# Kernel optimization log

Measured on AMD Instinct MI355X. Metric: run time of the kernel, lower is better.

## Reference

```python
import jax, jax.numpy as jnp
import numpy as np

VOCAB, EMBED, ZCH = 4096, 128, 256
B, H, W = 32, 16, 16


def setup_inputs() -> dict:
    key = jax.random.key(0)
    k1, k2, k3, k4 = jax.random.split(key, 4)
    z_e = jax.random.normal(k1, (B, ZCH, H, W), dtype=jnp.float32)
    pre_w = jax.random.normal(k2, (EMBED, ZCH), dtype=jnp.float32) * 0.02
    pre_b = jnp.zeros((EMBED,), dtype=jnp.float32)
    # codebook initialized uniform(-1/vocab, 1/vocab) like the torch module
    emb = jax.random.uniform(k3, (VOCAB, EMBED), dtype=jnp.float32,
                             minval=-1.0 / VOCAB, maxval=1.0 / VOCAB)
    post_w = jax.random.normal(k4, (ZCH, EMBED), dtype=jnp.float32) * 0.02
    post_b = jnp.zeros((ZCH,), dtype=jnp.float32)
    return {"z_e": z_e, "pre_w": pre_w, "pre_b": pre_b, "emb": emb,
            "post_w": post_w, "post_b": post_b}


def reference(z_e, pre_w, pre_b, emb, post_w, post_b):
    # pre_quant_conv: 1x1 conv == per-pixel linear, z_channels -> embed_dim
    z = jnp.einsum('bchw,ec->behw', z_e, pre_w) + pre_b[None, :, None, None]
    b, e, h, w = z.shape
    zf = z.transpose(0, 2, 3, 1).reshape(-1, e)                 # (b*h*w, e)
    # squared distance to all codebook vectors: |z|^2 + |c|^2 - 2 z.c
    dist = (jnp.sum(zf * zf, axis=1, keepdims=True)
            + jnp.sum(emb * emb, axis=1)
            - 2.0 * zf @ emb.T)                                  # (b*h*w, vocab)
    tokens = jnp.argmin(dist, axis=-1)                           # (b*h*w,)
    z_q = emb[tokens].reshape(b, h, w, e).transpose(0, 3, 1, 2)  # (b,e,h,w)
    # straight-through estimator
    dec_in = z + jax.lax.stop_gradient(z_q - z)
    # post_quant_conv: 1x1 conv embed_dim -> z_channels (decoder input)
    rec = jnp.einsum('behw,ce->bchw', dec_in, post_w) + post_b[None, :, None, None]
    return z, z_q, rec
```

## Files before the change

### kernel.cpp

```cpp
#include <hip/hip_runtime.h>
#include <hip/hip_bf16.h>
#include <cstdint>

#define NB   32
#define NC   256
#define NE   128
#define NS   256
#define NV   4096
#define NP   8192
#define NSPLIT 8

typedef unsigned short ushort_t;
typedef __attribute__((ext_vector_type(8))) short bf16x8;
typedef __attribute__((ext_vector_type(8))) unsigned short us8;
typedef __attribute__((ext_vector_type(4))) float f32x4;

__device__ __forceinline__ float bf2f(ushort_t u) {
    union { unsigned int i; float f; } x; x.i = ((unsigned int)u) << 16; return x.f;
}
__device__ __forceinline__ ushort_t f2bf(float f) {
    __hip_bfloat16 h = __float2bfloat16(f);
    ushort_t u; __builtin_memcpy(&u, &h, 2); return u;
}
__device__ __forceinline__ unsigned asu(float f) { unsigned u; __builtin_memcpy(&u,&f,4); return u; }
__device__ __forceinline__ float    asf(unsigned u) { float f; __builtin_memcpy(&f,&u,4); return f; }

__global__ __launch_bounds__(256) void pre_conv_pack(
    const float* __restrict__ z_e, const float* __restrict__ pre_w,
    const float* __restrict__ pre_b, const float* __restrict__ emb,
    float* __restrict__ out_z, ushort_t* __restrict__ Bpack,
    float* __restrict__ cnorm)
{
    __shared__ __align__(16) float wtile[16 * 256];
    __shared__ __align__(16) float part[4 * 16 * 64];

    const int t = threadIdx.x;

    if (blockIdx.x == 8) {
        const int v     = (blockIdx.y * 4 + blockIdx.z) * 32 + (t >> 3);
        const int chunk = t & 7;
        const float4* rp = (const float4*)(emb + (size_t)v * NE + chunk * 16);
        float4 x0 = rp[0], x1 = rp[1], x2 = rp[2], x3 = rp[3];
        float xs[16] = { x0.x, x0.y, x0.z, x0.w, x1.x, x1.y, x1.z, x1.w,
                         x2.x, x2.y, x2.z, x2.w, x3.x, x3.y, x3.z, x3.w };
        us8 h0, h1;
        float nn = 0.f;
#pragma unroll
        for (int j = 0; j < 8; j++) {
            nn = fmaf(xs[j], xs[j], nn);
            h0[j] = f2bf(xs[j]);
        }
#pragma unroll
        for (int j = 0; j < 8; j++) {
            nn = fmaf(xs[8 + j], xs[8 + j], nn);
            h1[j] = f2bf(xs[8 + j]);
        }
        nn += __shfl_xor(nn, 1);
        nn += __shfl_xor(nn, 2);
        nn += __shfl_xor(nn, 4);
        if (chunk == 0) cnorm[v] = 0.5f * nn;

        const int G  = v >> 4;
        const int ks = chunk >> 1;
        const int q0 = (chunk & 1) * 2;
        const int L0 = (v & 15) | (q0 << 4);
        const int L1 = (v & 15) | ((q0 + 1) << 4);
        *(us8*)(Bpack + ((size_t)G * 4 + ks) * 512 + L0 * 8) = h0;
        *(us8*)(Bpack + ((size_t)G * 4 + ks) * 512 + L1 * 8) = h1;
        return;
    }

    const int e0 = blockIdx.x * 16;
    const int b  = blockIdx.y;
    const int s0 = blockIdx.z * 64;

    for (int idx = t; idx < 16 * 256; idx += 256)
        wtile[idx] = pre_w[(e0 + (idx >> 8)) * 256 + (idx & 255)];
    __syncthreads();

    const int kq = t >> 6, sl = t & 63;
    float acc[16];
#pragma unroll
    for (int r = 0; r < 16; r++) acc[r] = 0.f;

    const float* zin = z_e + (size_t)(b * NC + kq * 64) * NS + s0 + sl;
    const int cb = kq * 64;
#pragma unroll 4
    for (int i = 0; i < 16; i++) {
        const int c = i * 4;
        float z0 = zin[(c + 0) * NS];
        float z1 = zin[(c + 1) * NS];
        float z2 = zin[(c + 2) * NS];
        float z3 = zin[(c + 3) * NS];
#pragma unroll
        for (int r = 0; r < 16; r++) {
            float4 w = *(const float4*)&wtile[r * 256 + cb + c];
            acc[r] = fmaf(z0, w.x, fmaf(z1, w.y, fmaf(z2, w.z, fmaf(z3, w.w, acc[r]))));
        }
    }
#pragma unroll
    for (int r = 0; r < 16; r++)
        part[(kq * 16 + r) * 64 + sl] = acc[r];
    __syncthreads();

    const int r4 = t >> 6, sl2 = t & 63;
#pragma unroll
    for (int j = 0; j < 4; j++) {
        const int r = j * 4 + r4;
        float v = pre_b[e0 + r]
                + part[(0 * 16 + r) * 64 + sl2]
                + part[(1 * 16 + r) * 64 + sl2]
                + part[(2 * 16 + r) * 64 + sl2]
                + part[(3 * 16 + r) * 64 + sl2];
        out_z[(size_t)(b * NE + e0 + r) * NS + s0 + sl2] = v;
    }
}

__global__ __launch_bounds__(256, 3) void score_mfma(
    const float* __restrict__ z, const ushort_t* __restrict__ Bpack,
    const float* __restrict__ cnorm, int* __restrict__ pidx4)
{
    __shared__ __align__(16) char smraw[40960];
    float* As  = (float*)smraw;
    float* r1  = (float*)smraw;
    float* r2  = (float*)(smraw + 16640);
    float* t4b = (float*)(smraw + 33280);

    const int t = threadIdx.x;
    const int wave = t >> 6, lane = t & 63;
    const int set = blockIdx.x;
    const int split = blockIdx.y;
    const int p0 = set * 64;
    const int b  = p0 >> 8;
    const int s0 = p0 & 255;

    for (int idx = t; idx < 64 * 128; idx += 256) {
        int k = idx >> 6, i = idx & 63;
        As[i * 132 + k] = z[(size_t)(b * NE + k) * NS + s0 + i];
    }
    __syncthreads();

    const int am = lane & 15, aq = lane >> 4;
    bf16x8 ah[4][4];
#pragma unroll
    for (int mt = 0; mt < 4; mt++)
#pragma unroll
        for (int ks = 0; ks < 4; ks++) {
            const unsigned* src = (const unsigned*)(As + (mt * 16 + am) * 132 + ks * 32 + aq * 8);
            union { unsigned u[4]; bf16x8 v; } pk;
#pragma unroll
            for (int pr = 0; pr < 4; pr++)
                pk.u[pr] = (src[2 * pr + 1] & 0xFFFF0000u) | (src[2 * pr] >> 16);
            ah[mt][ks] = pk.v;
        }
    __syncthreads();

    const int Gbase = split * 32 + wave * 8;
    float cn[8];
#pragma unroll
    for (int cgi = 0; cgi < 8; cgi++)
        cn[cgi] = cnorm[(Gbase + cgi) * 16 + am];

    float b1v[16], b2v[16];
#pragma unroll
    for (int i = 0; i < 16; i++) { b1v[i] = -1e30f; b2v[i] = -1e30f; }

    bf16x8 bh[4], bhn[4];
#pragma unroll
    for (int ks = 0; ks < 4; ks++)
        bh[ks] = *(const bf16x8*)(Bpack + ((size_t)Gbase * 4 + ks) * 512 + lane * 8);

    for (int cgi = 0; cgi < 8; cgi++) {
        if (cgi < 7) {
#pragma unroll
            for (int ks = 0; ks < 4; ks++)
                bhn[ks] = *(const bf16x8*)(Bpack + ((size_t)(Gbase + cgi + 1) * 4 + ks) * 512 + lane * 8);
        }

        f32x4 acc[4];
#pragma unroll
        for (int mt = 0; mt < 4; mt++) acc[mt] = (f32x4){0.f, 0.f, 0.f, 0.f};
#pragma unroll
        for (int ks = 0; ks < 4; ks++)
#pragma unroll
            for (int mt = 0; mt < 4; mt++)
                acc[mt] = __builtin_amdgcn_mfma_f32_16x16x32_bf16(ah[mt][ks], bh[ks], acc[mt], 0, 0, 0);

#pragma unroll
        for (int mt = 0; mt < 4; mt++)
#pragma unroll
            for (int reg = 0; reg < 4; reg++) {
                const int si = mt * 4 + reg;
                float sc = acc[mt][reg] - cn[cgi];
                float ev = asf((asu(sc) & ~7u) | (unsigned)cgi);
                b2v[si] = fmaxf(b2v[si], fminf(ev, b1v[si]));
                b1v[si] = fmaxf(b1v[si], ev);
            }
#pragma unroll
        for (int ks = 0; ks < 4; ks++) bh[ks] = bhn[ks];
    }

    const int slot = wave * 16 + am;
#pragma unroll
    for (int mt = 0; mt < 4; mt++)
#pragma unroll
        for (int reg = 0; reg < 4; reg++) {
            int px = mt * 16 + aq * 4 + reg;
            r1[slot * 65 + px] = b1v[mt * 4 + reg];
            r2[slot * 65 + px] = b2v[mt * 4 + reg];
        }
    __syncthreads();

    {
        const int px = t >> 2, ch = t & 3;
        float t1 = -1e30f, t2 = -1e30f, t3 = -1e30f, t4 = -1e30f;
        for (int i = 0; i < 16; i++) {
            int sl = ch * 16 + i;
#pragma unroll
            for (int e = 0; e < 2; e++) {
                float raw = e ? r2[sl * 65 + px] : r1[sl * 65 + px];
                unsigned vb = asu(raw);
                float v = asf((vb & ~511u) | ((unsigned)sl << 3) | (vb & 7u));
                t4 = fmaxf(t4, fminf(v, t3));
                t3 = fmaxf(t3, fminf(v, t2));
                t2 = fmaxf(t2, fminf(v, t1));
                t1 = fmaxf(t1, v);
            }
        }
        float* dst = t4b + (px * 4 + ch) * 4;
        dst[0] = t1; dst[1] = t2; dst[2] = t3; dst[3] = t4;
    }
    __syncthreads();

    if (t < 64) {
        float u1 = -1e30f, u2 = -1e30f, u3 = -1e30f, u4 = -1e30f;
        for (int ch = 0; ch < 4; ch++) {
#pragma unroll
            for (int j = 0; j < 4; j++) {
                float v = t4b[(t * 4 + ch) * 4 + j];
                u4 = fmaxf(u4, fminf(v, u3));
                u3 = fmaxf(u3, fminf(v, u2));
                u2 = fmaxf(u2, fminf(v, u1));
                u1 = fmaxf(u1, v);
            }
        }
        const int p = p0 + t;
        float uu[4] = { u1, u2, u3, u4 };
#pragma unroll
        for (int j = 0; j < 4; j++) {
            unsigned bits = asu(uu[j]) & 511u;
            int w = (int)(bits >> 7), res = (int)((bits >> 3) & 15u), cg = (int)(bits & 7u);
            pidx4[((size_t)split * NP + p) * 4 + j] = split * 512 + (w * 8 + cg) * 16 + res;
        }
    }
}

__global__ __launch_bounds__(512, 4) void rescore_gather_post2(
    const float* __restrict__ z, const float* __restrict__ emb,
    const int* __restrict__ pidx4, const float* __restrict__ post_w,
    const float* __restrict__ post_b, float* __restrict__ out_zq,
    float* __restrict__ out_rec)
{
    __shared__ __align__(16) float zl[16 * 132];
    __shared__ __align__(16) float eg[16 * 132];
    __shared__ int tok[16];

    const int t  = threadIdx.x;
    const int p0 = blockIdx.x * 16;
    const int b  = p0 >> 8;
    const int s0 = p0 & 255;

    for (int idx = t; idx < 16 * 128; idx += 512) {
        int k = idx >> 4, i = idx & 15;
        zl[i * 132 + k] = z[(size_t)(b * NE + k) * NS + s0 + i];
    }
    __syncthreads();

    {
        const int il = t >> 5;
        const int cc = t & 31;
        const int p  = p0 + il;
        const int split = cc >> 2, slot = cc & 3;
        const int idx = pidx4[((size_t)split * NP + p) * 4 + slot];
        const float* er = emb + (size_t)idx * NE;
        const float* zr = &zl[il * 132];

        double d0 = 0.0, d1 = 0.0, d2 = 0.0, d3 = 0.0;
        double n0 = 0.0, n1 = 0.0, n2 = 0.0, n3 = 0.0;
#pragma unroll
        for (int k = 0; k < NE; k += 16) {
            float4 e0 = *(const float4*)(er + k + 0);
            float4 e1 = *(const float4*)(er + k + 4);
            float4 e2 = *(const float4*)(er + k + 8);
            float4 e3 = *(const float4*)(er + k + 12);
            float4 z0 = *(const float4*)(zr + k + 0);
            float4 z1 = *(const float4*)(zr + k + 4);
            float4 z2 = *(const float4*)(zr + k + 8);
            float4 z3 = *(const float4*)(zr + k + 12);
            d0 += (double)z0.x * e0.x; d0 += (double)z0.y * e0.y;
            d0 += (double)z0.z * e0.z; d0 += (double)z0.w * e0.w;
            d1 += (double)z1.x * e1.x; d1 += (double)z1.y * e1.y;
            d1 += (double)z1.z * e1.z; d1 += (double)z1.w * e1.w;
            d2 += (double)z2.x * e2.x; d2 += (double)z2.y * e2.y;
            d2 += (double)z2.z * e2.z; d2 += (double)z2.w * e2.w;
            d3 += (double)z3.x * e3.x; d3 += (double)z3.y * e3.y;
            d3 += (double)z3.z * e3.z; d3 += (double)z3.w * e3.w;
            n0 += (double)e0.x * e0.x; n0 += (double)e0.y * e0.y;
            n0 += (double)e0.z * e0.z; n0 += (double)e0.w * e0.w;
            n1 += (double)e1.x * e1.x; n1 += (double)e1.y * e1.y;
            n1 += (double)e1.z * e1.z; n1 += (double)e1.w * e1.w;
            n2 += (double)e2.x * e2.x; n2 += (double)e2.y * e2.y;
            n2 += (double)e2.z * e2.z; n2 += (double)e2.w * e2.w;
            n3 += (double)e3.x * e3.x; n3 += (double)e3.y * e3.y;
            n3 += (double)e3.z * e3.z; n3 += (double)e3.w * e3.w;
        }
        double bs = ((d0 + d1) + (d2 + d3)) - 0.5 * ((n0 + n1) + (n2 + n3));
        int bi = idx;
#pragma unroll
        for (int m = 1; m <= 16; m <<= 1) {
            double osc = __shfl_xor(bs, m);
            int    obi = __shfl_xor(bi, m);
            if (osc > bs || (osc == bs && obi < bi)) { bs = osc; bi = obi; }
        }
        if (cc == 0) tok[il] = bi;
    }
    __syncthreads();

    for (int idx = t; idx < NE * 16; idx += 512) {
        int e = idx >> 4, i = idx & 15;
        float v = emb[(size_t)tok[i] * NE + e];
        out_zq[(size_t)(b * NE + e) * NS + s0 + i] = v;
        eg[i * 132 + e] = v;
    }
    __syncthreads();

    {
        const int c  = t & 255;
        const int ph = t >> 8;
        const int pb = ph * 8;
        const float* wr = post_w + (size_t)c * NE;

        float a0 = 0.f, a1 = 0.f, a2 = 0.f, a3 = 0.f;
        float a4 = 0.f, a5 = 0.f, a6 = 0.f, a7 = 0.f;
#pragma unroll 4
        for (int k = 0; k < NE; k += 4) {
            float4 w4 = *(const float4*)(wr + k);
            float4 q;
            q = *(const float4*)&eg[(pb + 0) * 132 + k];
            a0 = fmaf(w4.x, q.x, fmaf(w4.y, q.y, fmaf(w4.z, q.z, fmaf(w4.w, q.w, a0))));
            q = *(const float4*)&eg[(pb + 1) * 132 + k];
            a1 = fmaf(w4.x, q.x, fmaf(w4.y, q.y, fmaf(w4.z, q.z, fmaf(w4.w, q.w, a1))));
            q = *(const float4*)&eg[(pb + 2) * 132 + k];
            a2 = fmaf(w4.x, q.x, fmaf(w4.y, q.y, fmaf(w4.z, q.z, fmaf(w4.w, q.w, a2))));
            q = *(const float4*)&eg[(pb + 3) * 132 + k];
            a3 = fmaf(w4.x, q.x, fmaf(w4.y, q.y, fmaf(w4.z, q.z, fmaf(w4.w, q.w, a3))));
            q = *(const float4*)&eg[(pb + 4) * 132 + k];
            a4 = fmaf(w4.x, q.x, fmaf(w4.y, q.y, fmaf(w4.z, q.z, fmaf(w4.w, q.w, a4))));
            q = *(const float4*)&eg[(pb + 5) * 132 + k];
            a5 = fmaf(w4.x, q.x, fmaf(w4.y, q.y, fmaf(w4.z, q.z, fmaf(w4.w, q.w, a5))));
            q = *(const float4*)&eg[(pb + 6) * 132 + k];
            a6 = fmaf(w4.x, q.x, fmaf(w4.y, q.y, fmaf(w4.z, q.z, fmaf(w4.w, q.w, a6))));
            q = *(const float4*)&eg[(pb + 7) * 132 + k];
            a7 = fmaf(w4.x, q.x, fmaf(w4.y, q.y, fmaf(w4.z, q.z, fmaf(w4.w, q.w, a7))));
        }
        const float bias = post_b[c];
        float4 lo = { a0 + bias, a1 + bias, a2 + bias, a3 + bias };
        float4 hi = { a4 + bias, a5 + bias, a6 + bias, a7 + bias };
        float* dst = out_rec + (size_t)(b * NC + c) * NS + s0 + pb;
        *(float4*)(dst + 0) = lo;
        *(float4*)(dst + 4) = hi;
    }
}

extern "C" void kernel_launch(void* const* d_in, const int* in_sizes, int n_in,
                              void* d_out, int out_size, void* d_ws, size_t ws_size,
                              hipStream_t stream)
{
    const float* z_e    = (const float*)d_in[0];
    const float* pre_w  = (const float*)d_in[1];
    const float* pre_b  = (const float*)d_in[2];
    const float* emb    = (const float*)d_in[3];
    const float* post_w = (const float*)d_in[4];
    const float* post_b = (const float*)d_in[5];

    float* out     = (float*)d_out;
    float* out_z   = out;
    float* out_zq  = out + 1048576;
    float* out_rec = out + 2097152;

    const size_t SZ_BPACK = (size_t)256 * 4 * 512 * 2;
    const size_t SZ_CNORM = (size_t)NV * 4;
    const size_t SZ_PIDX4 = (size_t)NSPLIT * NP * 4 * 4;
    const size_t NEED = SZ_BPACK + SZ_CNORM + SZ_PIDX4;
    char* scr = (ws_size >= NEED) ? (char*)d_ws : (char*)out_rec;
    ushort_t* Bpack = (ushort_t*)scr;
    float*    cnorm = (float*)(scr + SZ_BPACK);
    int*      pidx4 = (int*)(scr + SZ_BPACK + SZ_CNORM);

    pre_conv_pack       <<<dim3(9, 32, 4),    256, 0, stream>>>(z_e, pre_w, pre_b, emb,
                                                                out_z, Bpack, cnorm);
    score_mfma          <<<dim3(128, NSPLIT), 256, 0, stream>>>(out_z, Bpack, cnorm, pidx4);
    rescore_gather_post2<<<dim3(512),         512, 0, stream>>>(out_z, emb, pidx4,
                                                                post_w, post_b,
                                                                out_zq, out_rec);
}
```

Before: 152.9 us.

## Fuse pre-conv, codebook scoring, rescoring and post-conv into one per-tile kernel

Replaces the three-kernel pipeline with a small codebook-packing kernel and one fused kernel per 32-pixel tile. That kernel computes the pre-conv into shared memory, runs the bf16 MFMA scoring over all codebook splits in sequence, reduces the top-4 candidates per split in shared memory, rescores them in double precision, gathers, and applies the post-conv. It removes the global round trips of z and the candidate buffer and two launches. The cost is only 256 blocks, each looping serially over all 4096 codes, so parallelism across the GPU drops.

Measured after the change: 144.4 us. -5.5%, faster.

```diff
diff --git a/kernel.cpp b/kernel.cpp
--- a/kernel.cpp
+++ b/kernel.cpp
@@ -15,9 +15,6 @@
 typedef __attribute__((ext_vector_type(8))) unsigned short us8;
 typedef __attribute__((ext_vector_type(4))) float f32x4;
 
-__device__ __forceinline__ float bf2f(ushort_t u) {
-    union { unsigned int i; float f; } x; x.i = ((unsigned int)u) << 16; return x.f;
-}
 __device__ __forceinline__ ushort_t f2bf(float f) {
     __hip_bfloat16 h = __float2bfloat16(f);
     ushort_t u; __builtin_memcpy(&u, &h, 2); return u;
@@ -25,299 +22,305 @@
 __device__ __forceinline__ unsigned asu(float f) { unsigned u; __builtin_memcpy(&u,&f,4); return u; }
 __device__ __forceinline__ float    asf(unsigned u) { float f; __builtin_memcpy(&f,&u,4); return f; }
 
-__global__ __launch_bounds__(256) void pre_conv_pack(
+__global__ __launch_bounds__(256) void pack_emb(
+    const float* __restrict__ emb, ushort_t* __restrict__ Bpack,
+    float* __restrict__ cnorm)
+{
+    const int t = threadIdx.x;
+    const int v     = blockIdx.x * 32 + (t >> 3);
+    const int chunk = t & 7;
+    const float4* rp = (const float4*)(emb + (size_t)v * NE + chunk * 16);
+    float4 x0 = rp[0], x1 = rp[1], x2 = rp[2], x3 = rp[3];
+    float xs[16] = { x0.x, x0.y, x0.z, x0.w, x1.x, x1.y, x1.z, x1.w,
+                     x2.x, x2.y, x2.z, x2.w, x3.x, x3.y, x3.z, x3.w };
+    us8 h0, h1;
+    float nn = 0.f;
+#pragma unroll
+    for (int j = 0; j < 8; j++) {
+        nn = fmaf(xs[j], xs[j], nn);
+        h0[j] = f2bf(xs[j]);
+    }
+#pragma unroll
+    for (int j = 0; j < 8; j++) {
+        nn = fmaf(xs[8 + j], xs[8 + j], nn);
+        h1[j] = f2bf(xs[8 + j]);
+    }
+    nn += __shfl_xor(nn, 1);
+    nn += __shfl_xor(nn, 2);
+    nn += __shfl_xor(nn, 4);
+    if (chunk == 0) cnorm[v] = 0.5f * nn;
+
+    const int G  = v >> 4;
+    const int ks = chunk >> 1;
+    const int q0 = (chunk & 1) * 2;
+    const int L0 = (v & 15) | (q0 << 4);
+    const int L1 = (v & 15) | ((q0 + 1) << 4);
+    *(us8*)(Bpack + ((size_t)G * 4 + ks) * 512 + L0 * 8) = h0;
+    *(us8*)(Bpack + ((size_t)G * 4 + ks) * 512 + L1 * 8) = h1;
+}
+
+#define ZE_STR  36
+#define ZL_STR  132
+#define ZE_OFF  0
+#define R1_OFF  0
+#define R2_OFF  16896
+#define ZL_OFF  36864
+#define T4B_OFF 53760
+#define CAND_OFF 57856
+#define TOK_OFF 61952
+#define SM_SIZE 62080
+
+__global__ __launch_bounds__(512, 2) void vq_main(
     const float* __restrict__ z_e, const float* __restrict__ pre_w,
     const float* __restrict__ pre_b, const float* __restrict__ emb,
-    float* __restrict__ out_z, ushort_t* __restrict__ Bpack,
-    float* __restrict__ cnorm)
+    const float* __restrict__ post_w, const float* __restrict__ post_b,
+    const ushort_t* __restrict__ Bpack, const float* __restrict__ cnorm,
+    float* __restrict__ out_z, float* __restrict__ out_zq,
+    float* __restrict__ out_rec)
 {
-    __shared__ __align__(16) float wtile[16 * 256];
-    __shared__ __align__(16) float part[4 * 16 * 64];
-
-    const int t = threadIdx.x;
-
-    if (blockIdx.x == 8) {
-        const int v     = (blockIdx.y * 4 + blockIdx.z) * 32 + (t >> 3);
-        const int chunk = t & 7;
-        const float4* rp = (const float4*)(emb + (size_t)v * NE + chunk * 16);
-        float4 x0 = rp[0], x1 = rp[1], x2 = rp[2], x3 = rp[3];
-        float xs[16] = { x0.x, x0.y, x0.z, x0.w, x1.x, x1.y, x1.z, x1.w,
-                         x2.x, x2.y, x2.z, x2.w, x3.x, x3.y, x3.z, x3.w };
-        us8 h0, h1;
-        float nn = 0.f;
-#pragma unroll
-        for (int j = 0; j < 8; j++) {
-            nn = fmaf(xs[j], xs[j], nn);
-            h0[j] = f2bf(xs[j]);
-        }
-#pragma unroll
-        for (int j = 0; j < 8; j++) {
-            nn = fmaf(xs[8 + j], xs[8 + j], nn);
-            h1[j] = f2bf(xs[8 + j]);
-        }
-        nn += __shfl_xor(nn, 1);
-        nn += __shfl_xor(nn, 2);
-        nn += __shfl_xor(nn, 4);
-        if (chunk == 0) cnorm[v] = 0.5f * nn;
-
-        const int G  = v >> 4;
-        const int ks = chunk >> 1;
-        const int q0 = (chunk & 1) * 2;
-        const int L0 = (v & 15) | (q0 << 4);
-        const int L1 = (v & 15) | ((q0 + 1) << 4);
-        *(us8*)(Bpack + ((size_t)G * 4 + ks) * 512 + L0 * 8) = h0;
-        *(us8*)(Bpack + ((size_t)G * 4 + ks) * 512 + L1 * 8) = h1;
-        return;
-    }
-
-    const int e0 = blockIdx.x * 16;
-    const int b  = blockIdx.y;
-    const int s0 = blockIdx.z * 64;
-
-    for (int idx = t; idx < 16 * 256; idx += 256)
-        wtile[idx] = pre_w[(e0 + (idx >> 8)) * 256 + (idx & 255)];
+    __shared__ __align__(16) char smraw[SM_SIZE];
+    float* ze   = (float*)(smraw + ZE_OFF);
+    float* r1   = (float*)(smraw + R1_OFF);
+    float* r2   = (float*)(smraw + R2_OFF);
+    float* zl   = (float*)(smraw + ZL_OFF);
+    float* eg   = (float*)(smraw + ZL_OFF);
+    float* t4b  = (float*)(smraw + T4B_OFF);
+    int*   cand = (int*)(smraw + CAND_OFF);
+    int*   tok  = (int*)(smraw + TOK_OFF);
+
+    const int t  = threadIdx.x;
+    const int b  = blockIdx.x >> 3;
+    const int s0 = (blockIdx.x & 7) * 32;
+
+    for (int idx = t; idx < NC * 32; idx += 512) {
+        int c = idx >> 5, i = idx & 31;
+        ze[c * ZE_STR + i] = z_e[((size_t)b * NC + c) * NS + s0 + i];
+    }
     __syncthreads();
 
-    const int kq = t >> 6, sl = t & 63;
-    float acc[16];
-#pragma unroll
-    for (int r = 0; r < 16; r++) acc[r] = 0.f;
-
-    const float* zin = z_e + (size_t)(b * NC + kq * 64) * NS + s0 + sl;
-    const int cb = kq * 64;
-#pragma unroll 4
-    for (int i = 0; i < 16; i++) {
-        const int c = i * 4;
-        float z0 = zin[(c + 0) * NS];
-        float z1 = zin[(c + 1) * NS];
-        float z2 = zin[(c + 2) * NS];
-        float z3 = zin[(c + 3) * NS];
-#pragma unroll
-        for (int r = 0; r < 16; r++) {
-            float4 w = *(const float4*)&wtile[r * 256 + cb + c];
-            acc[r] = fmaf(z0, w.x, fmaf(z1, w.y, fmaf(z2, w.z, fmaf(z3, w.w, acc[r]))));
-        }
-    }
-#pragma unroll
-    for (int r = 0; r < 16; r++)
-        part[(kq * 16 + r) * 64 + sl] = acc[r];
+    {
+        const int pg = t >> 7;
+        const int e  = t & 127;
+        const float* wr = pre_w + (size_t)e * NC;
+        float a0 = 0.f, a1 = 0.f, a2 = 0.f, a3 = 0.f;
+        float a4 = 0.f, a5 = 0.f, a6 = 0.f, a7 = 0.f;
+#pragma unroll 2
+        for (int c = 0; c < NC; c += 4) {
+            float4 w4 = *(const float4*)(wr + c);
+            float4 za, zb;
+            za = *(const float4*)&ze[(c + 0) * ZE_STR + pg * 8];
+            zb = *(const float4*)&ze[(c + 0) * ZE_STR + pg * 8 + 4];
+            a0 = fmaf(w4.x, za.x, a0); a1 = fmaf(w4.x, za.y, a1);
+            a2 = fmaf(w4.x, za.z, a2); a3 = fmaf(w4.x, za.w, a3);
+            a4 = fmaf(w4.x, zb.x, a4); a5 = fmaf(w4.x, zb.y, a5);
+            a6 = fmaf(w4.x, zb.z, a6); a7 = fmaf(w4.x, zb.w, a7);
+            za = *(const float4*)&ze[(c + 1) * ZE_STR + pg * 8];
+            zb = *(const float4*)&ze[(c + 1) * ZE_STR + pg * 8 + 4];
+            a0 = fmaf(w4.y, za.x, a0); a1 = fmaf(w4.y, za.y, a1);
+            a2 = fmaf(w4.y, za.z, a2); a3 = fmaf(w4.y, za.w, a3);
+            a4 = fmaf(w4.y, zb.x, a4); a5 = fmaf(w4.y, zb.y, a5);
+            a6 = fmaf(w4.y, zb.z, a6); a7 = fmaf(w4.y, zb.w, a7);
+            za = *(const float4*)&ze[(c + 2) * ZE_STR + pg * 8];
+            zb = *(const float4*)&ze[(c + 2) * ZE_STR + pg * 8 + 4];
+            a0 = fmaf(w4.z, za.x, a0); a1 = fmaf(w4.z, za.y, a1);
+            a2 = fmaf(w4.z, za.z, a2); a3 = fmaf(w4.z, za.w, a3);
+            a4 = fmaf(w4.z, zb.x, a4); a5 = fmaf(w4.z, zb.y, a5);
+            a6 = fmaf(w4.z, zb.z, a6); a7 = fmaf(w4.z, zb.w, a7);
+            za = *(const float4*)&ze[(c + 3) * ZE_STR + pg * 8];
+            zb = *(const float4*)&ze[(c + 3) * ZE_STR + pg * 8 + 4];
+            a0 = fmaf(w4.w, za.x, a0); a1 = fmaf(w4.w, za.y, a1);
+            a2 = fmaf(w4.w, za.z, a2); a3 = fmaf(w4.w, za.w, a3);
+            a4 = fmaf(w4.w, zb.x, a4); a5 = fmaf(w4.w, zb.y, a5);
+            a6 = fmaf(w4.w, zb.z, a6); a7 = fmaf(w4.w, zb.w, a7);
+        }
+        const float bias = pre_b[e];
+        a0 += bias; a1 += bias; a2 += bias; a3 += bias;
+        a4 += bias; a5 += bias; a6 += bias; a7 += bias;
+        zl[(pg * 8 + 0) * ZL_STR + e] = a0;
+        zl[(pg * 8 + 1) * ZL_STR + e] = a1;
+        zl[(pg * 8 + 2) * ZL_STR + e] = a2;
+        zl[(pg * 8 + 3) * ZL_STR + e] = a3;
+        zl[(pg * 8 + 4) * ZL_STR + e] = a4;
+        zl[(pg * 8 + 5) * ZL_STR + e] = a5;
+        zl[(pg * 8 + 6) * ZL_STR + e] = a6;
+        zl[(pg * 8 + 7) * ZL_STR + e] = a7;
+        float4 lo = { a0, a1, a2, a3 };
+        float4 hi = { a4, a5, a6, a7 };
+        float* dst = out_z + ((size_t)b * NE + e) * NS + s0 + pg * 8;
+        *(float4*)(dst + 0) = lo;
+        *(float4*)(dst + 4) = hi;
+    }
     __syncthreads();
 
-    const int r4 = t >> 6, sl2 = t & 63;
-#pragma unroll
-    for (int j = 0; j < 4; j++) {
-        const int r = j * 4 + r4;
-        float v = pre_b[e0 + r]
-                + part[(0 * 16 + r) * 64 + sl2]
-                + part[(1 * 16 + r) * 64 + sl2]
-                + part[(2 * 16 + r) * 64 + sl2]
-                + part[(3 * 16 + r) * 64 + sl2];
-        out_z[(size_t)(b * NE + e0 + r) * NS + s0 + sl2] = v;
-    }
-}
-
-__global__ __launch_bounds__(256, 3) void score_mfma(
-    const float* __restrict__ z, const ushort_t* __restrict__ Bpack,
-    const float* __restrict__ cnorm, int* __restrict__ pidx4)
-{
-    __shared__ __align__(16) char smraw[40960];
-    float* As  = (float*)smraw;
-    float* r1  = (float*)smraw;
-    float* r2  = (float*)(smraw + 16640);
-    float* t4b = (float*)(smraw + 33280);
-
-    const int t = threadIdx.x;
     const int wave = t >> 6, lane = t & 63;
-    const int set = blockIdx.x;
-    const int split = blockIdx.y;
-    const int p0 = set * 64;
-    const int b  = p0 >> 8;
-    const int s0 = p0 & 255;
-
-    for (int idx = t; idx < 64 * 128; idx += 256) {
-        int k = idx >> 6, i = idx & 63;
-        As[i * 132 + k] = z[(size_t)(b * NE + k) * NS + s0 + i];
-    }
-    __syncthreads();
-
     const int am = lane & 15, aq = lane >> 4;
-    bf16x8 ah[4][4];
-#pragma unroll
-    for (int mt = 0; mt < 4; mt++)
+
+    bf16x8 ah[2][4];
+#pragma unroll
+    for (int mt = 0; mt < 2; mt++)
 #pragma unroll
         for (int ks = 0; ks < 4; ks++) {
-            const unsigned* src = (const unsigned*)(As + (mt * 16 + am) * 132 + ks * 32 + aq * 8);
+            const unsigned* src = (const unsigned*)(zl + (mt * 16 + am) * ZL_STR + ks * 32 + aq * 8);
             union { unsigned u[4]; bf16x8 v; } pk;
 #pragma unroll
             for (int pr = 0; pr < 4; pr++)
                 pk.u[pr] = (src[2 * pr + 1] & 0xFFFF0000u) | (src[2 * pr] >> 16);
             ah[mt][ks] = pk.v;
         }
-    __syncthreads();
-
-    const int Gbase = split * 32 + wave * 8;
-    float cn[8];
-#pragma unroll
-    for (int cgi = 0; cgi < 8; cgi++)
-        cn[cgi] = cnorm[(Gbase + cgi) * 16 + am];
-
-    float b1v[16], b2v[16];
-#pragma unroll
-    for (int i = 0; i < 16; i++) { b1v[i] = -1e30f; b2v[i] = -1e30f; }
-
-    bf16x8 bh[4], bhn[4];
-#pragma unroll
-    for (int ks = 0; ks < 4; ks++)
-        bh[ks] = *(const bf16x8*)(Bpack + ((size_t)Gbase * 4 + ks) * 512 + lane * 8);
-
-    for (int cgi = 0; cgi < 8; cgi++) {
-        if (cgi < 7) {
+
+    const int wq = wave >> 2;
+    const int wv = wave & 3;
+
+    for (int sp = 0; sp < NSPLIT; sp += 2) {
+        const int split = sp + wq;
+        const int Gbase = split * 32 + wv * 8;
+        float cn[8];
+#pragma unroll
+        for (int cgi = 0; cgi < 8; cgi++)
+            cn[cgi] = cnorm[(Gbase + cgi) * 16 + am];
+
+        float b1v[8], b2v[8];
+#pragma unroll
+        for (int i = 0; i < 8; i++) { b1v[i] = -1e30f; b2v[i] = -1e30f; }
+
+        bf16x8 bh[4], bhn[4];
+#pragma unroll
+        for (int ks = 0; ks < 4; ks++)
+            bh[ks] = *(const bf16x8*)(Bpack + ((size_t)Gbase * 4 + ks) * 512 + lane * 8);
+
+        for (int cgi = 0; cgi < 8; cgi++) {
+            if (cgi < 7) {
+#pragma unroll
+                for (int ks = 0; ks < 4; ks++)
+                    bhn[ks] = *(const bf16x8*)(Bpack + ((size_t)(Gbase + cgi + 1) * 4 + ks) * 512 + lane * 8);
+            }
+            f32x4 acc[2];
+#pragma unroll
+            for (int mt = 0; mt < 2; mt++) acc[mt] = (f32x4){0.f, 0.f, 0.f, 0.f};
 #pragma unroll
             for (int ks = 0; ks < 4; ks++)
-                bhn[ks] = *(const bf16x8*)(Bpack + ((size_t)(Gbase + cgi + 1) * 4 + ks) * 512 + lane * 8);
-        }
-
-        f32x4 acc[4];
-#pragma unroll
-        for (int mt = 0; mt < 4; mt++) acc[mt] = (f32x4){0.f, 0.f, 0.f, 0.f};
-#pragma unroll
-        for (int ks = 0; ks < 4; ks++)
-#pragma unroll
-            for (int mt = 0; mt < 4; mt++)
-                acc[mt] = __builtin_amdgcn_mfma_f32_16x16x32_bf16(ah[mt][ks], bh[ks], acc[mt], 0, 0, 0);
-
-#pragma unroll
-        for (int mt = 0; mt < 4; mt++)
+#pragma unroll
+                for (int mt = 0; mt < 2; mt++)
+                    acc[mt] = __builtin_amdgcn_mfma_f32_16x16x32_bf16(ah[mt][ks], bh[ks], acc[mt], 0, 0, 0);
+
+#pragma unroll
+            for (int mt = 0; mt < 2; mt++)
+#pragma unroll
+                for (int reg = 0; reg < 4; reg++) {
+                    const int si = mt * 4 + reg;
+                    float sc = acc[mt][reg] - cn[cgi];
+                    float ev = asf((asu(sc) & ~7u) | (unsigned)cgi);
+                    b2v[si] = fmaxf(b2v[si], fminf(ev, b1v[si]));
+                    b1v[si] = fmaxf(b1v[si], ev);
+                }
+#pragma unroll
+            for (int ks = 0; ks < 4; ks++) bh[ks] = bhn[ks];
+        }
+
+        const int slot = wv * 16 + am;
+#pragma unroll
+        for (int mt = 0; mt < 2; mt++)
 #pragma unroll
             for (int reg = 0; reg < 4; reg++) {
-                const int si = mt * 4 + reg;
-                float sc = acc[mt][reg] - cn[cgi];
-                float ev = asf((asu(sc) & ~7u) | (unsigned)cgi);
-                b2v[si] = fmaxf(b2v[si], fminf(ev, b1v[si]));
-                b1v[si] = fmaxf(b1v[si], ev);
-            }
-#pragma unroll
-        for (int ks = 0; ks < 4; ks++) bh[ks] = bhn[ks];
-    }
-
-    const int slot = wave * 16 + am;
-#pragma unroll
-    for (int mt = 0; mt < 4; mt++)
-#pragma unroll
-        for (int reg = 0; reg < 4; reg++) {
-            int px = mt * 16 + aq * 4 + reg;
-            r1[slot * 65 + px] = b1v[mt * 4 + reg];
-            r2[slot * 65 + px] = b2v[mt * 4 + reg];
-        }
-    __syncthreads();
+                int px = mt * 16 + aq * 4 + reg;
+                r1[(wq * 64 + slot) * 33 + px] = b1v[mt * 4 + reg];
+                r2[(wq * 64 + slot) * 33 + px] = b2v[mt * 4 + reg];
+            }
+        __syncthreads();
+
+        if (t < 256) {
+            const int wq2 = t >> 7, rem = t & 127;
+            const int px = rem >> 2, ch = rem & 3;
+            float t1 = -1e30f, t2 = -1e30f, t3 = -1e30f, t4 = -1e30f;
+            for (int i = 0; i < 16; i++) {
+                int sl = ch * 16 + i;
+#pragma unroll
+                for (int e = 0; e < 2; e++) {
+                    float raw = e ? r2[(wq2 * 64 + sl) * 33 + px]
+                                  : r1[(wq2 * 64 + sl) * 33 + px];
+                    unsigned vb = asu(raw);
+                    float v = asf((vb & ~511u) | ((unsigned)sl << 3) | (vb & 7u));
+                    t4 = fmaxf(t4, fminf(v, t3));
+                    t3 = fmaxf(t3, fminf(v, t2));
+                    t2 = fmaxf(t2, fminf(v, t1));
+                    t1 = fmaxf(t1, v);
+                }
+            }
+            float* dst = t4b + ((wq2 * 32 + px) * 4 + ch) * 4;
+            dst[0] = t1; dst[1] = t2; dst[2] = t3; dst[3] = t4;
+        }
+        __syncthreads();
+
+        if (t < 64) {
+            const int wq2 = t >> 5, px = t & 31;
+            float u1 = -1e30f, u2 = -1e30f, u3 = -1e30f, u4 = -1e30f;
+            for (int ch = 0; ch < 4; ch++) {
+#pragma unroll
+                for (int j = 0; j < 4; j++) {
+                    float v = t4b[((wq2 * 32 + px) * 4 + ch) * 4 + j];
+                    u4 = fmaxf(u4, fminf(v, u3));
+                    u3 = fmaxf(u3, fminf(v, u2));
+                    u2 = fmaxf(u2, fminf(v, u1));
+                    u1 = fmaxf(u1, v);
+                }
+            }
+            const int spw = sp + wq2;
+            float uu[4] = { u1, u2, u3, u4 };
+#pragma unroll
+            for (int j = 0; j < 4; j++) {
+                unsigned bits = asu(uu[j]) & 511u;
+                int w = (int)(bits >> 7), res = (int)((bits >> 3) & 15u), cg = (int)(bits & 7u);
+                cand[(spw * 32 + px) * 4 + j] = spw * 512 + (w * 8 + cg) * 16 + res;
+            }
+        }
+        __syncthreads();
+    }
 
     {
-        const int px = t >> 2, ch = t & 3;
-        float t1 = -1e30f, t2 = -1e30f, t3 = -1e30f, t4 = -1e30f;
-        for (int i = 0; i < 16; i++) {
-            int sl = ch * 16 + i;
-#pragma unroll
-            for (int e = 0; e < 2; e++) {
-                float raw = e ? r2[sl * 65 + px] : r1[sl * 65 + px];
-                unsigned vb = asu(raw);
-                float v = asf((vb & ~511u) | ((unsigned)sl << 3) | (vb & 7u));
-                t4 = fmaxf(t4, fminf(v, t3));
-                t3 = fmaxf(t3, fminf(v, t2));
-                t2 = fmaxf(t2, fminf(v, t1));
-                t1 = fmaxf(t1, v);
-            }
-        }
-        float* dst = t4b + (px * 4 + ch) * 4;
-        dst[0] = t1; dst[1] = t2; dst[2] = t3; dst[3] = t4;
-    }
-    __syncthreads();
-
-    if (t < 64) {
-        float u1 = -1e30f, u2 = -1e30f, u3 = -1e30f, u4 = -1e30f;
-        for (int ch = 0; ch < 4; ch++) {
-#pragma unroll
-            for (int j = 0; j < 4; j++) {
-                float v = t4b[(t * 4 + ch) * 4 + j];
-                u4 = fmaxf(u4, fminf(v, u3));
-                u3 = fmaxf(u3, fminf(v, u2));
-                u2 = fmaxf(u2, fminf(v, u1));
-                u1 = fmaxf(u1, v);
-            }
-        }
-        const int p = p0 + t;
-        float uu[4] = { u1, u2, u3, u4 };
-#pragma unroll
-        for (int j = 0; j < 4; j++) {
-            unsigned bits = asu(uu[j]) & 511u;
-            int w = (int)(bits >> 7), res = (int)((bits >> 3) & 15u), cg = (int)(bits & 7u);
-            pidx4[((size_t)split * NP + p) * 4 + j] = split * 512 + (w * 8 + cg) * 16 + res;
-        }
-    }
-}
-
-__global__ __launch_bounds__(512, 4) void rescore_gather_post2(
-    const float* __restrict__ z, const float* __restrict__ emb,
-    const int* __restrict__ pidx4, const float* __restrict__ post_w,
-    const float* __restrict__ post_b, float* __restrict__ out_zq,
-    float* __restrict__ out_rec)
-{
-    __shared__ __align__(16) float zl[16 * 132];
-    __shared__ __align__(16) float eg[16 * 132];
-    __shared__ int tok[16];
-
-    const int t  = threadIdx.x;
-    const int p0 = blockIdx.x * 16;
-    const int b  = p0 >> 8;
-    const int s0 = p0 & 255;
-
-    for (int idx = t; idx < 16 * 128; idx += 512) {
-        int k = idx >> 4, i = idx & 15;
-        zl[i * 132 + k] = z[(size_t)(b * NE + k) * NS + s0 + i];
-    }
-    __syncthreads();
-
-    {
-        const int il = t >> 5;
-        const int cc = t & 31;
-        const int p  = p0 + il;
-        const int split = cc >> 2, slot = cc & 3;
-        const int idx = pidx4[((size_t)split * NP + p) * 4 + slot];
-        const float* er = emb + (size_t)idx * NE;
-        const float* zr = &zl[il * 132];
-
-        double d0 = 0.0, d1 = 0.0, d2 = 0.0, d3 = 0.0;
-        double n0 = 0.0, n1 = 0.0, n2 = 0.0, n3 = 0.0;
-#pragma unroll
-        for (int k = 0; k < NE; k += 16) {
-            float4 e0 = *(const float4*)(er + k + 0);
-            float4 e1 = *(const float4*)(er + k + 4);
-            float4 e2 = *(const float4*)(er + k + 8);
-            float4 e3 = *(const float4*)(er + k + 12);
-            float4 z0 = *(const float4*)(zr + k + 0);
-            float4 z1 = *(const float4*)(zr + k + 4);
-            float4 z2 = *(const float4*)(zr + k + 8);
-            float4 z3 = *(const float4*)(zr + k + 12);
-            d0 += (double)z0.x * e0.x; d0 += (double)z0.y * e0.y;
-            d0 += (double)z0.z * e0.z; d0 += (double)z0.w * e0.w;
-            d1 += (double)z1.x * e1.x; d1 += (double)z1.y * e1.y;
-            d1 += (double)z1.z * e1.z; d1 += (double)z1.w * e1.w;
-            d2 += (double)z2.x * e2.x; d2 += (double)z2.y * e2.y;
-            d2 += (double)z2.z * e2.z; d2 += (double)z2.w * e2.w;
-            d3 += (double)z3.x * e3.x; d3 += (double)z3.y * e3.y;
-            d3 += (double)z3.z * e3.z; d3 += (double)z3.w * e3.w;
-            n0 += (double)e0.x * e0.x; n0 += (double)e0.y * e0.y;
-            n0 += (double)e0.z * e0.z; n0 += (double)e0.w * e0.w;
-            n1 += (double)e1.x * e1.x; n1 += (double)e1.y * e1.y;
-            n1 += (double)e1.z * e1.z; n1 += (double)e1.w * e1.w;
-            n2 += (double)e2.x * e2.x; n2 += (double)e2.y * e2.y;
-            n2 += (double)e2.z * e2.z; n2 += (double)e2.w * e2.w;
-            n3 += (double)e3.x * e3.x; n3 += (double)e3.y * e3.y;
-            n3 += (double)e3.z * e3.z; n3 += (double)e3.w * e3.w;
-        }
-        double bs = ((d0 + d1) + (d2 + d3)) - 0.5 * ((n0 + n1) + (n2 + n3));
-        int bi = idx;
-#pragma unroll
-        for (int m = 1; m <= 16; m <<= 1) {
+        const int il = t >> 4;
+        const int cc = t & 15;
+        double bs = -1e300; int bi = 0x7fffffff;
+        const float* zr = zl + il * ZL_STR;
+#pragma unroll
+        for (int jj = 0; jj < 2; jj++) {
+            int c2 = cc * 2 + jj;
+            int split = c2 >> 2, slot = c2 & 3;
+            int idx = cand[(split * 32 + il) * 4 + slot];
+            const float* er = emb + (size_t)idx * NE;
+            double d0 = 0.0, d1 = 0.0, d2 = 0.0, d3 = 0.0;
+            double n0 = 0.0, n1 = 0.0, n2 = 0.0, n3 = 0.0;
+#pragma unroll
+            for (int k = 0; k < NE; k += 16) {
+                float4 e0 = *(const float4*)(er + k + 0);
+                float4 e1 = *(const float4*)(er + k + 4);
+                float4 e2 = *(const float4*)(er + k + 8);
+                float4 e3 = *(const float4*)(er + k + 12);
+                float4 z0 = *(const float4*)(zr + k + 0);
+                float4 z1 = *(const float4*)(zr + k + 4);
+                float4 z2 = *(const float4*)(zr + k + 8);
+                float4 z3 = *(const float4*)(zr + k + 12);
+                d0 += (double)z0.x * e0.x; d0 += (double)z0.y * e0.y;
+                d0 += (double)z0.z * e0.z; d0 += (double)z0.w * e0.w;
+                d1 += (double)z1.x * e1.x; d1 += (double)z1.y * e1.y;
+                d1 += (double)z1.z * e1.z; d1 += (double)z1.w * e1.w;
+                d2 += (double)z2.x * e2.x; d2 += (double)z2.y * e2.y;
+                d2 += (double)z2.z * e2.z; d2 += (double)z2.w * e2.w;
+                d3 += (double)z3.x * e3.x; d3 += (double)z3.y * e3.y;
+                d3 += (double)z3.z * e3.z; d3 += (double)z3.w * e3.w;
+                n0 += (double)e0.x * e0.x; n0 += (double)e0.y * e0.y;
+                n0 += (double)e0.z * e0.z; n0 += (double)e0.w * e0.w;
+                n1 += (double)e1.x * e1.x; n1 += (double)e1.y * e1.y;
+                n1 += (double)e1.z * e1.z; n1 += (double)e1.w * e1.w;
+                n2 += (double)e2.x * e2.x; n2 += (double)e2.y * e2.y;
+                n2 += (double)e2.z * e2.z; n2 += (double)e2.w * e2.w;
+                n3 += (double)e3.x * e3.x; n3 += (double)e3.y * e3.y;
+                n3 += (double)e3.z * e3.z; n3 += (double)e3.w * e3.w;
+            }
+            double sc = ((d0 + d1) + (d2 + d3)) - 0.5 * ((n0 + n1) + (n2 + n3));
+            if (sc > bs || (sc == bs && idx < bi)) { bs = sc; bi = idx; }
+        }
+#pragma unroll
+        for (int m = 1; m <= 8; m <<= 1) {
             double osc = __shfl_xor(bs, m);
             int    obi = __shfl_xor(bi, m);
             if (osc > bs || (osc == bs && obi < bi)) { bs = osc; bi = obi; }
@@ -326,49 +329,55 @@
     }
     __syncthreads();
 
-    for (int idx = t; idx < NE * 16; idx += 512) {
-        int e = idx >> 4, i = idx & 15;
-        float v = emb[(size_t)tok[i] * NE + e];
-        out_zq[(size_t)(b * NE + e) * NS + s0 + i] = v;
-        eg[i * 132 + e] = v;
+    for (int idx = t; idx < 32 * 32; idx += 512) {
+        int px = idx >> 5, eq = idx & 31;
+        float4 v4 = *(const float4*)(emb + (size_t)tok[px] * NE + eq * 4);
+        *(float4*)&eg[px * ZL_STR + eq * 4] = v4;
+    }
+    __syncthreads();
+    for (int idx = t; idx < NE * 32; idx += 512) {
+        int e = idx >> 5, i = idx & 31;
+        out_zq[((size_t)b * NE + e) * NS + s0 + i] = eg[i * ZL_STR + e];
     }
     __syncthreads();
 
     {
         const int c  = t & 255;
         const int ph = t >> 8;
-        const int pb = ph * 8;
         const float* wr = post_w + (size_t)c * NE;
-
-        float a0 = 0.f, a1 = 0.f, a2 = 0.f, a3 = 0.f;
-        float a4 = 0.f, a5 = 0.f, a6 = 0.f, a7 = 0.f;
+        const float bias = post_b[c];
+#pragma unroll
+        for (int pass = 0; pass < 2; pass++) {
+            const int pb = pass * 16 + ph * 8;
+            float a0 = 0.f, a1 = 0.f, a2 = 0.f, a3 = 0.f;
+            float a4 = 0.f, a5 = 0.f, a6 = 0.f, a7 = 0.f;
 #pragma unroll 4
-        for (int k = 0; k < NE; k += 4) {
-            float4 w4 = *(const float4*)(wr + k);
-            float4 q;
-            q = *(const float4*)&eg[(pb + 0) * 132 + k];
-            a0 = fmaf(w4.x, q.x, fmaf(w4.y, q.y, fmaf(w4.z, q.z, fmaf(w4.w, q.w, a0))));
-            q = *(const float4*)&eg[(pb + 1) * 132 + k];
-            a1 = fmaf(w4.x, q.x, fmaf(w4.y, q.y, fmaf(w4.z, q.z, fmaf(w4.w, q.w, a1))));
-            q = *(const float4*)&eg[(pb + 2) * 132 + k];
-            a2 = fmaf(w4.x, q.x, fmaf(w4.y, q.y, fmaf(w4.z, q.z, fmaf(w4.w, q.w, a2))));
-            q = *(const float4*)&eg[(pb + 3) * 132 + k];
-            a3 = fmaf(w4.x, q.x, fmaf(w4.y, q.y, fmaf(w4.z, q.z, fmaf(w4.w, q.w, a3))));
-            q = *(const float4*)&eg[(pb + 4) * 132 + k];
-            a4 = fmaf(w4.x, q.x, fmaf(w4.y, q.y, fmaf(w4.z, q.z, fmaf(w4.w, q.w, a4))));
-            q = *(const float4*)&eg[(pb + 5) * 132 + k];
-            a5 = fmaf(w4.x, q.x, fmaf(w4.y, q.y, fmaf(w4.z, q.z, fmaf(w4.w, q.w, a5))));
-            q = *(const float4*)&eg[(pb + 6) * 132 + k];
-            a6 = fmaf(w4.x, q.x, fmaf(w4.y, q.y, fmaf(w4.z, q.z, fmaf(w4.w, q.w, a6))));
-            q = *(const float4*)&eg[(pb + 7) * 132 + k];
-            a7 = fmaf(w4.x, q.x, fmaf(w4.y, q.y, fmaf(w4.z, q.z, fmaf(w4.w, q.w, a7))));
-        }
-        const float bias = post_b[c];
-        float4 lo = { a0 + bias, a1 + bias, a2 + bias, a3 + bias };
-        float4 hi = { a4 + bias, a5 + bias, a6 + bias, a7 + bias };
-        float* dst = out_rec + (size_t)(b * NC + c) * NS + s0 + pb;
-        *(float4*)(dst + 0) = lo;
-        *(float4*)(dst + 4) = hi;
+            for (int k = 0; k < NE; k += 4) {
+                float4 w4 = *(const float4*)(wr + k);
+                float4 q;
+                q = *(const float4*)&eg[(pb + 0) * ZL_STR + k];
+                a0 = fmaf(w4.x, q.x, fmaf(w4.y, q.y, fmaf(w4.z, q.z, fmaf(w4.w, q.w, a0))));
+                q = *(const float4*)&eg[(pb + 1) * ZL_STR + k];
+                a1 = fmaf(w4.x, q.x, fmaf(w4.y, q.y, fmaf(w4.z, q.z, fmaf(w4.w, q.w, a1))));
+                q = *(const float4*)&eg[(pb + 2) * ZL_STR + k];
+                a2 = fmaf(w4.x, q.x, fmaf(w4.y, q.y, fmaf(w4.z, q.z, fmaf(w4.w, q.w, a2))));
+                q = *(const float4*)&eg[(pb + 3) * ZL_STR + k];
+                a3 = fmaf(w4.x, q.x, fmaf(w4.y, q.y, fmaf(w4.z, q.z, fmaf(w4.w, q.w, a3))));
+                q = *(const float4*)&eg[(pb + 4) * ZL_STR + k];
+                a4 = fmaf(w4.x, q.x, fmaf(w4.y, q.y, fmaf(w4.z, q.z, fmaf(w4.w, q.w, a4))));
+                q = *(const float4*)&eg[(pb + 5) * ZL_STR + k];
+                a5 = fmaf(w4.x, q.x, fmaf(w4.y, q.y, fmaf(w4.z, q.z, fmaf(w4.w, q.w, a5))));
+                q = *(const float4*)&eg[(pb + 6) * ZL_STR + k];
+                a6 = fmaf(w4.x, q.x, fmaf(w4.y, q.y, fmaf(w4.z, q.z, fmaf(w4.w, q.w, a6))));
+                q = *(const float4*)&eg[(pb + 7) * ZL_STR + k];
+                a7 = fmaf(w4.x, q.x, fmaf(w4.y, q.y, fmaf(w4.z, q.z, fmaf(w4.w, q.w, a7))));
+            }
+            float4 lo = { a0 + bias, a1 + bias, a2 + bias, a3 + bias };
+            float4 hi = { a4 + bias, a5 + bias, a6 + bias, a7 + bias };
+            float* dst = out_rec + ((size_t)b * NC + c) * NS + s0 + pb;
+            *(float4*)(dst + 0) = lo;
+            *(float4*)(dst + 4) = hi;
+        }
     }
 }
 
@@ -390,17 +399,13 @@
 
     const size_t SZ_BPACK = (size_t)256 * 4 * 512 * 2;
     const size_t SZ_CNORM = (size_t)NV * 4;
-    const size_t SZ_PIDX4 = (size_t)NSPLIT * NP * 4 * 4;
-    const size_t NEED = SZ_BPACK + SZ_CNORM + SZ_PIDX4;
+    const size_t NEED = SZ_BPACK + SZ_CNORM;
     char* scr = (ws_size >= NEED) ? (char*)d_ws : (char*)out_rec;
     ushort_t* Bpack = (ushort_t*)scr;
     float*    cnorm = (float*)(scr + SZ_BPACK);
-    int*      pidx4 = (int*)(scr + SZ_BPACK + SZ_CNORM);
-
-    pre_conv_pack       <<<dim3(9, 32, 4),    256, 0, stream>>>(z_e, pre_w, pre_b, emb,
-                                                                out_z, Bpack, cnorm);
-    score_mfma          <<<dim3(128, NSPLIT), 256, 0, stream>>>(out_z, Bpack, cnorm, pidx4);
-    rescore_gather_post2<<<dim3(512),         512, 0, stream>>>(out_z, emb, pidx4,
-                                                                post_w, post_b,
-                                                                out_zq, out_rec);
+
+    pack_emb<<<dim3(128), 256, 0, stream>>>(emb, Bpack, cnorm);
+    vq_main <<<dim3(256), 512, 0, stream>>>(z_e, pre_w, pre_b, emb,
+                                            post_w, post_b, Bpack, cnorm,
+                                            out_z, out_zq, out_rec);
 }
```
